# Performance work log

Hardware: AMD Instinct MI355X
Metric: run time of the kernel (lower is better)

Reference implementation:

```python
import jax, jax.numpy as jnp
import numpy as np

EMBED_DIM = 1024
NUM_HEADS = 16
HEAD_DIM = EMBED_DIM // NUM_HEADS  # 64
KV_RANK = 64
QK_RANK = 64
EPS = 1e-6


def rmsnorm(x, w):
    var = jnp.mean(x * x, axis=-1, keepdims=True)
    return x * jax.lax.rsqrt(var + EPS) * w


def setup_inputs() -> dict:
    key = jax.random.key(0)
    ks = jax.random.split(key, 6)
    B, N, C = 4, 2048, EMBED_DIM
    s = lambda fan_in: 1.0 / np.sqrt(fan_in)
    return {
        "x": jax.random.normal(ks[0], (B, N, C), dtype=jnp.float32),
        # nn.Linear weights stored as [out_features, in_features]
        "w_kv_a": jax.random.normal(ks[1], (KV_RANK, C), dtype=jnp.float32) * s(C),
        "w_kv_b": jax.random.normal(ks[2], (NUM_HEADS * HEAD_DIM * 2, KV_RANK), dtype=jnp.float32) * s(KV_RANK),
        "w_q_a": jax.random.normal(ks[3], (QK_RANK, C), dtype=jnp.float32) * s(C),
        "w_q_b": jax.random.normal(ks[4], (NUM_HEADS * HEAD_DIM, QK_RANK), dtype=jnp.float32) * s(QK_RANK),
        "w_proj": jax.random.normal(ks[5], (C, NUM_HEADS * HEAD_DIM), dtype=jnp.float32) * s(NUM_HEADS * HEAD_DIM),
        "kv_norm_w": jnp.ones((KV_RANK,), dtype=jnp.float32),
        "q_norm_w": jnp.ones((QK_RANK,), dtype=jnp.float32),
    }


def reference(x, w_kv_a, w_kv_b, w_q_a, w_q_b, w_proj, kv_norm_w, q_norm_w):
    B, N, C = x.shape
    H, D = NUM_HEADS, HEAD_DIM
    scale = D ** -0.5

    # low-rank KV path
    kv_latent = rmsnorm(x @ w_kv_a.T, kv_norm_w)              # [B,N,r]
    kv = (kv_latent @ w_kv_b.T).reshape(B, N, H, 2, D)
    k = kv[:, :, :, 0, :].transpose(0, 2, 1, 3)               # [B,H,N,D]
    v = kv[:, :, :, 1, :].transpose(0, 2, 1, 3)               # [B,H,N,D]

    # low-rank Q path
    q_latent = rmsnorm(x @ w_q_a.T, q_norm_w)                 # [B,N,r]
    q = (q_latent @ w_q_b.T).reshape(B, N, H, D).transpose(0, 2, 1, 3)

    attn = jnp.einsum("bhqd,bhkd->bhqk", q, k) * scale        # [B,H,N,N]
    attn = jax.nn.softmax(attn, axis=-1)
    y = jnp.einsum("bhqk,bhkd->bhqd", attn, v)                # [B,H,N,D]

    y = y.transpose(0, 2, 1, 3).reshape(B, N, H * D)
    return y @ w_proj.T
```

## Files before the change

kernel.cpp:

```cpp
#include <hip/hip_runtime.h>
#include <stdint.h>

typedef __bf16 bf16;
typedef __bf16 bf16x8 __attribute__((ext_vector_type(8)));
typedef __bf16 bf16x4 __attribute__((ext_vector_type(4)));
typedef float  f32x4  __attribute__((ext_vector_type(4)));

#define MFMA16(a,b,c) __builtin_amdgcn_mfma_f32_16x16x32_bf16((a),(b),(c),0,0,0)
#define LOG2E 1.44269504f

__device__ __forceinline__ void gl16(const bf16* g, bf16* l) {
  __builtin_amdgcn_global_load_lds((const __attribute__((address_space(1))) void*)g,
                                   (__attribute__((address_space(3))) void*)l, 16, 0, 0);
}

#define OFF_XB     0LL
#define OFF_WAB    8388608LL
#define OFF_WKVB   8519680LL
#define OFF_WQB    8650752LL
#define OFF_WPROJ  8716288LL
#define OFF_LATN   9764864LL
#define OFF_K      10813440LL
#define OFF_VT     19202048LL
#define OFF_Q      27590656LL
#define OFF_Y      35979264LL

__global__ __launch_bounds__(256) void k_convert(
    const float* __restrict__ x, const float* __restrict__ wkva, const float* __restrict__ wkvb,
    const float* __restrict__ wqa, const float* __restrict__ wqb, const float* __restrict__ wproj,
    bf16* __restrict__ ws)
{
  int64_t q = (int64_t)blockIdx.x * 256 + threadIdx.x;
  const float* src; bf16* dst;
  if (q < 2097152LL)      { src = x + 4*q;                          dst = ws + OFF_XB + 4*q; }
  else if (q < 2129920LL) { int64_t e = 4*(q - 2097152LL);
                            int row = (int)(e >> 10), col = (int)(e & 1023);
                            src = (row < 64) ? (wkva + ((int64_t)row << 10) + col)
                                             : (wqa + ((int64_t)(row - 64) << 10) + col);
                            dst = ws + OFF_WAB + e; }
  else if (q < 2162688LL) { int64_t j = q - 2129920LL; src = wkvb + 4*j; dst = ws + OFF_WKVB + 4*j; }
  else if (q < 2179072LL) { int64_t j = q - 2162688LL; src = wqb  + 4*j; dst = ws + OFF_WQB  + 4*j; }
  else if (q < 2441216LL) { int64_t j = q - 2179072LL; src = wproj+ 4*j; dst = ws + OFF_WPROJ+ 4*j; }
  else return;
  float4 v = *(const float4*)src;
  bf16x4 o; o.x = (bf16)v.x; o.y = (bf16)v.y; o.z = (bf16)v.z; o.w = (bf16)v.w;
  *(bf16x4*)dst = o;
}

__device__ __forceinline__ void gemm_core(
    const bf16* __restrict__ A, const bf16* __restrict__ B,
    int lda, int ldb, int K, int m0, int n0,
    bf16* As, bf16* Bs, f32x4 acc[4][4])
{
  const int tid = threadIdx.x, lane = tid & 63;
  const int wr = tid >> 7, wc = (tid >> 6) & 1;
  const int r0 = tid >> 3, c0 = (tid & 7) * 8;
  const int csw = (((tid & 7) ^ (r0 & 7)) * 8);
  const int fr = lane & 15, fg = lane >> 4;
#pragma unroll
  for (int mi = 0; mi < 4; mi++)
#pragma unroll
    for (int ni = 0; ni < 4; ni++) acc[mi][ni] = (f32x4){0.f, 0.f, 0.f, 0.f};
  for (int kt = 0; kt < K; kt += 64) {
#pragma unroll
    for (int p = 0; p < 4; p++) {
      int row = p * 32 + r0;
      gl16(A + (int64_t)(m0 + row) * lda + kt + csw, As + row * 64 + c0);
      gl16(B + (int64_t)(n0 + row) * ldb + kt + csw, Bs + row * 64 + c0);
    }
    __syncthreads();
#pragma unroll
    for (int kk = 0; kk < 2; kk++) {
      bf16x8 af[4], bfr[4];
#pragma unroll
      for (int i = 0; i < 4; i++) {
        af[i]  = *(const bf16x8*)(As + (wr * 64 + i * 16 + fr) * 64 + (((kk * 4 + fg) ^ (fr & 7)) * 8));
        bfr[i] = *(const bf16x8*)(Bs + (wc * 64 + i * 16 + fr) * 64 + (((kk * 4 + fg) ^ (fr & 7)) * 8));
      }
#pragma unroll
      for (int mi = 0; mi < 4; mi++)
#pragma unroll
        for (int ni = 0; ni < 4; ni++)
          acc[mi][ni] = MFMA16(af[mi], bfr[ni], acc[mi][ni]);
    }
    __syncthreads();
  }
}

__global__ __launch_bounds__(256, 2) void k_latent(
    const bf16* __restrict__ xb, const bf16* __restrict__ wab,
    const float* __restrict__ kvw, const float* __restrict__ qw,
    bf16* __restrict__ latn)
{
  __shared__ bf16 As[128 * 64], Bs[128 * 64];
  f32x4 acc[4][4];
  const int m0 = blockIdx.x * 128;
  gemm_core(xb, wab, 1024, 1024, 1024, m0, 0, As, Bs, acc);
  const int tid = threadIdx.x, lane = tid & 63, wr = tid >> 7, wc = (tid >> 6) & 1;
  const int fr = lane & 15, fg = lane >> 4;
  const float* nw = wc ? qw : kvw;
  float wv[4];
#pragma unroll
  for (int ni = 0; ni < 4; ni++) wv[ni] = nw[ni * 16 + fr];
#pragma unroll
  for (int mi = 0; mi < 4; mi++) {
    f32x4 ss;
#pragma unroll
    for (int r = 0; r < 4; r++) {
      float s = 0.f;
#pragma unroll
      for (int ni = 0; ni < 4; ni++) { float v = acc[mi][ni][r]; s += v * v; }
      ss[r] = s;
    }
#pragma unroll
    for (int mask = 1; mask < 16; mask <<= 1)
#pragma unroll
      for (int r = 0; r < 4; r++) ss[r] += __shfl_xor(ss[r], mask, 64);
    f32x4 sc;
#pragma unroll
    for (int r = 0; r < 4; r++) sc[r] = rsqrtf(ss[r] * (1.f / 64.f) + 1e-6f);
#pragma unroll
    for (int ni = 0; ni < 4; ni++)
#pragma unroll
      for (int r = 0; r < 4; r++) {
        int row = m0 + wr * 64 + mi * 16 + fg * 4 + r;
        latn[(int64_t)row * 128 + wc * 64 + ni * 16 + fr] = (bf16)(acc[mi][ni][r] * sc[r] * wv[ni]);
      }
  }
}

__global__ __launch_bounds__(256, 2) void k_kv(
    const bf16* __restrict__ latn, const bf16* __restrict__ wkvb,
    bf16* __restrict__ kb, bf16* __restrict__ vtb)
{
  __shared__ bf16 As[128 * 64], Bs[128 * 64];
  f32x4 acc[4][4];
  const int m0 = blockIdx.x * 128, h = blockIdx.y;
  gemm_core(latn, wkvb, 128, 64, 64, m0, h * 128, As, Bs, acc);
  const int tid = threadIdx.x, lane = tid & 63, wr = tid >> 7, wc = (tid >> 6) & 1;
  const int fr = lane & 15, fg = lane >> 4;
#pragma unroll
  for (int mi = 0; mi < 4; mi++)
#pragma unroll
    for (int ni = 0; ni < 4; ni++)
#pragma unroll
      for (int r = 0; r < 4; r++) {
        int m = m0 + wr * 64 + mi * 16 + fg * 4 + r;
        int b = m >> 11, t = m & 2047;
        int c = ni * 16 + fr;
        bf16 v = (bf16)acc[mi][ni][r];
        if (wc == 0) kb [(int64_t)((b * 16 + h) * 2048 + t) * 64 + c] = v;
        else         vtb[(int64_t)((b * 16 + h) * 64 + c) * 2048 + t] = v;
      }
}

__global__ __launch_bounds__(256, 2) void k_q(
    const bf16* __restrict__ latn, const bf16* __restrict__ wqb,
    bf16* __restrict__ qbuf)
{
  __shared__ bf16 As[128 * 64], Bs[128 * 64];
  f32x4 acc[4][4];
  const int m0 = blockIdx.x * 128, n0 = blockIdx.y * 128;
  gemm_core(latn + 64, wqb, 128, 64, 64, m0, n0, As, Bs, acc);
  const int tid = threadIdx.x, lane = tid & 63, wr = tid >> 7, wc = (tid >> 6) & 1;
  const int fr = lane & 15, fg = lane >> 4;
#pragma unroll
  for (int mi = 0; mi < 4; mi++)
#pragma unroll
    for (int ni = 0; ni < 4; ni++)
#pragma unroll
      for (int r = 0; r < 4; r++) {
        int m = m0 + wr * 64 + mi * 16 + fg * 4 + r;
        int b = m >> 11, t = m & 2047;
        int n = n0 + wc * 64 + ni * 16 + fr;
        int hh = n >> 6, d = n & 63;
        qbuf[(int64_t)((b * 16 + hh) * 2048 + t) * 64 + d] = (bf16)(acc[mi][ni][r] * 0.125f);
      }
}

__global__ __launch_bounds__(256, 2) void k_attn(
    const bf16* __restrict__ qb, const bf16* __restrict__ kb,
    const bf16* __restrict__ vtb, bf16* __restrict__ yb)
{
  __shared__ bf16 Vts[64 * 64];
  __shared__ bf16 KsP[128 * 64];
  const int bh = blockIdx.x, qt = blockIdx.y;
  const int b = bh >> 4, h = bh & 15;
  const int tid = threadIdx.x, lane = tid & 63, w = tid >> 6;
  const int fr = lane & 15, fg = lane >> 4;
  const int fg4 = fg * 4;
  const int64_t base = (int64_t)bh * (2048 * 64);
  bf16* Ks = KsP;
  bf16* Pw = KsP + w * 32 * 64;
  const int q0 = qt * 128 + w * 32;

  bf16x8 aq[2][2];
#pragma unroll
  for (int mi = 0; mi < 2; mi++)
#pragma unroll
    for (int kk = 0; kk < 2; kk++)
      aq[mi][kk] = *(const bf16x8*)(qb + base + (int64_t)(q0 + mi * 16 + fr) * 64 + kk * 32 + fg * 8);

  f32x4 o[2][4];
  float mS[2], lS[2];
#pragma unroll
  for (int mi = 0; mi < 2; mi++) {
#pragma unroll
    for (int di = 0; di < 4; di++) o[mi][di] = (f32x4){0.f, 0.f, 0.f, 0.f};
    mS[mi] = -__builtin_inff(); lS[mi] = 0.f;
  }
  const int srow = tid >> 3, scol = tid & 7;

  for (int kt = 0; kt < 32; kt++) {
    const int t0 = kt * 64;
#pragma unroll
    for (int p = 0; p < 2; p++) {
      int row = p * 32 + srow;
      int csw = ((scol ^ (row & 7)) * 8);
      gl16(kb  + base + (int64_t)(t0 + row) * 64 + csw, Ks  + row * 64 + scol * 8);
      gl16(vtb + base + (int64_t)row * 2048 + t0 + csw, Vts + row * 64 + scol * 8);
    }
    __syncthreads();
    f32x4 sT[2][4];
#pragma unroll
    for (int mi = 0; mi < 2; mi++)
#pragma unroll
      for (int ni = 0; ni < 4; ni++) sT[mi][ni] = (f32x4){0.f, 0.f, 0.f, 0.f};
#pragma unroll
    for (int kk = 0; kk < 2; kk++) {
      bf16x8 bk[4];
#pragma unroll
      for (int ni = 0; ni < 4; ni++)
        bk[ni] = *(const bf16x8*)(Ks + (ni * 16 + fr) * 64 + (((kk * 4 + fg) ^ (fr & 7)) * 8));
#pragma unroll
      for (int mi = 0; mi < 2; mi++)
#pragma unroll
        for (int ni = 0; ni < 4; ni++)
          sT[mi][ni] = MFMA16(bk[ni], aq[mi][kk], sT[mi][ni]);
    }
    __syncthreads();
#pragma unroll
    for (int mi = 0; mi < 2; mi++) {
      float pm = sT[mi][0][0];
#pragma unroll
      for (int ni = 0; ni < 4; ni++)
#pragma unroll
        for (int r = 0; r < 4; r++) pm = fmaxf(pm, sT[mi][ni][r]);
      pm = fmaxf(pm, __shfl_xor(pm, 16, 64));
      pm = fmaxf(pm, __shfl_xor(pm, 32, 64));
      const bool grew = __any(pm > mS[mi]);
      float alphaS = 1.f;
      if (grew) {
        float mn = fmaxf(mS[mi], pm);
        alphaS = exp2f((mS[mi] - mn) * LOG2E);
        mS[mi] = mn;
      }
      const float mnL = mS[mi] * LOG2E;
      float rs = 0.f;
      bf16* pwr = Pw + (mi * 16 + fr) * 64 + (fg & 1) * 4;
      const int cxor = fr & 7;
#pragma unroll
      for (int ni = 0; ni < 4; ni++) {
        float p0 = exp2f(fmaf(sT[mi][ni][0], LOG2E, -mnL));
        float p1 = exp2f(fmaf(sT[mi][ni][1], LOG2E, -mnL));
        float p2 = exp2f(fmaf(sT[mi][ni][2], LOG2E, -mnL));
        float p3 = exp2f(fmaf(sT[mi][ni][3], LOG2E, -mnL));
        rs += (p0 + p1) + (p2 + p3);
        bf16x4 pk4;
        pk4[0] = (bf16)p0; pk4[1] = (bf16)p1; pk4[2] = (bf16)p2; pk4[3] = (bf16)p3;
        *(bf16x4*)(pwr + (((ni * 2 + (fg >> 1)) ^ cxor) << 3)) = pk4;
      }
      rs += __shfl_xor(rs, 16, 64);
      rs += __shfl_xor(rs, 32, 64);
      if (grew) {
        lS[mi] = lS[mi] * alphaS + rs;
        float aO[4];
#pragma unroll
        for (int r = 0; r < 4; r++) aO[r] = __shfl(alphaS, fg4 + r, 64);
#pragma unroll
        for (int di = 0; di < 4; di++)
#pragma unroll
          for (int r = 0; r < 4; r++) o[mi][di][r] *= aO[r];
      } else {
        lS[mi] += rs;
      }
    }
#pragma unroll
    for (int k2 = 0; k2 < 2; k2++) {
      bf16x8 pa[2], vv[4];
#pragma unroll
      for (int mi = 0; mi < 2; mi++)
        pa[mi] = *(const bf16x8*)(Pw + (mi * 16 + fr) * 64 + (((k2 * 4 + fg) ^ (fr & 7)) * 8));
#pragma unroll
      for (int di = 0; di < 4; di++)
        vv[di] = *(const bf16x8*)(Vts + (di * 16 + fr) * 64 + (((k2 * 4 + fg) ^ (fr & 7)) * 8));
#pragma unroll
      for (int mi = 0; mi < 2; mi++)
#pragma unroll
        for (int di = 0; di < 4; di++)
          o[mi][di] = MFMA16(pa[mi], vv[di], o[mi][di]);
    }
    __syncthreads();
  }
#pragma unroll
  for (int mi = 0; mi < 2; mi++) {
    float lO[4];
#pragma unroll
    for (int r = 0; r < 4; r++) lO[r] = __shfl(lS[mi], fg4 + r, 64);
#pragma unroll
    for (int di = 0; di < 4; di++)
#pragma unroll
      for (int r = 0; r < 4; r++) {
        int t = q0 + mi * 16 + fg * 4 + r;
        float v = o[mi][di][r] / lO[r];
        yb[((int64_t)b * 2048 + t) * 1024 + h * 64 + di * 16 + fr] = (bf16)v;
      }
  }
}

__global__ __launch_bounds__(256, 2) void k_proj(
    const bf16* __restrict__ yb, const bf16* __restrict__ wp, float* __restrict__ out)
{
  __shared__ bf16 As[128 * 64], Bs[128 * 64];
  f32x4 acc[4][4];
  const int m0 = blockIdx.x * 128, n0 = blockIdx.y * 128;
  gemm_core(yb, wp, 1024, 1024, 1024, m0, n0, As, Bs, acc);
  const int tid = threadIdx.x, lane = tid & 63, wr = tid >> 7, wc = (tid >> 6) & 1;
  const int fr = lane & 15, fg = lane >> 4;
#pragma unroll
  for (int mi = 0; mi < 4; mi++)
#pragma unroll
    for (int ni = 0; ni < 4; ni++)
#pragma unroll
      for (int r = 0; r < 4; r++) {
        int m = m0 + wr * 64 + mi * 16 + fg * 4 + r;
        int n = n0 + wc * 64 + ni * 16 + fr;
        out[(int64_t)m * 1024 + n] = acc[mi][ni][r];
      }
}

extern "C" void kernel_launch(void* const* d_in, const int* in_sizes, int n_in,
                              void* d_out, int out_size, void* d_ws, size_t ws_size,
                              hipStream_t stream) {
  (void)in_sizes; (void)n_in; (void)out_size; (void)ws_size;
  const float* x     = (const float*)d_in[0];
  const float* wkva  = (const float*)d_in[1];
  const float* wkvb  = (const float*)d_in[2];
  const float* wqa   = (const float*)d_in[3];
  const float* wqb   = (const float*)d_in[4];
  const float* wproj = (const float*)d_in[5];
  const float* kvw   = (const float*)d_in[6];
  const float* qw    = (const float*)d_in[7];
  bf16* ws  = (bf16*)d_ws;
  float* out = (float*)d_out;

  k_convert<<<dim3(9536), dim3(256), 0, stream>>>(x, wkva, wkvb, wqa, wqb, wproj, ws);
  k_latent <<<dim3(64), dim3(256), 0, stream>>>(ws + OFF_XB, ws + OFF_WAB, kvw, qw, ws + OFF_LATN);
  k_kv     <<<dim3(64, 16), dim3(256), 0, stream>>>(ws + OFF_LATN, ws + OFF_WKVB, ws + OFF_K, ws + OFF_VT);
  k_q      <<<dim3(64, 8), dim3(256), 0, stream>>>(ws + OFF_LATN, ws + OFF_WQB, ws + OFF_Q);
  k_attn   <<<dim3(64, 16), dim3(256), 0, stream>>>(ws + OFF_Q, ws + OFF_K, ws + OFF_VT, ws + OFF_Y);
  k_proj   <<<dim3(64, 8), dim3(256), 0, stream>>>(ws + OFF_Y, ws + OFF_WPROJ, out);
}
```

Baseline: 305.0 us.

## Double-buffer K/V tiles in attention and widen blocks to 8 waves

The attention kernel now prefetches the next K and V^T tile into a second LDS buffer while computing on the current one. Each block has 512 threads covering 256 queries, so every K/V tile in LDS is shared by more query rows. The P scratch gets its own dedicated buffer instead of aliasing the K tile, which removes one barrier per iteration. The cost is higher LDS use per block (about 64KB) and fewer blocks in the grid, with launch bounds raised to 512 threads and 4 blocks per CU, which may not be reachable.

```diff
diff --git a/kernel.cpp b/kernel.cpp
--- a/kernel.cpp
+++ b/kernel.cpp
@@ -178,21 +178,31 @@
       }
 }
 
-__global__ __launch_bounds__(256, 2) void k_attn(
+__global__ __launch_bounds__(512, 4) void k_attn(
     const bf16* __restrict__ qb, const bf16* __restrict__ kb,
     const bf16* __restrict__ vtb, bf16* __restrict__ yb)
 {
-  __shared__ bf16 Vts[64 * 64];
-  __shared__ bf16 KsP[128 * 64];
+  __shared__ bf16 Ks[2][64 * 64];
+  __shared__ bf16 Vts[2][64 * 64];
+  __shared__ bf16 Ps[8][32 * 64];
   const int bh = blockIdx.x, qt = blockIdx.y;
   const int b = bh >> 4, h = bh & 15;
   const int tid = threadIdx.x, lane = tid & 63, w = tid >> 6;
   const int fr = lane & 15, fg = lane >> 4;
   const int fg4 = fg * 4;
   const int64_t base = (int64_t)bh * (2048 * 64);
-  bf16* Ks = KsP;
-  bf16* Pw = KsP + w * 32 * 64;
-  const int q0 = qt * 128 + w * 32;
+  bf16* Pw = Ps[w];
+  const int q0 = qt * 256 + w * 32;
+
+  const int srow = tid >> 3, scol = tid & 7;
+  const int csw = ((scol ^ (srow & 7)) * 8);
+  const bf16* kSrc = kb  + base + (int64_t)srow * 64   + csw;
+  const bf16* vSrc = vtb + base + (int64_t)srow * 2048 + csw;
+  bf16* kD[2] = { &Ks[0][tid * 8],  &Ks[1][tid * 8]  };
+  bf16* vD[2] = { &Vts[0][tid * 8], &Vts[1][tid * 8] };
+
+  gl16(kSrc, kD[0]);
+  gl16(vSrc, vD[0]);
 
   bf16x8 aq[2][2];
 #pragma unroll
@@ -209,18 +219,19 @@
     for (int di = 0; di < 4; di++) o[mi][di] = (f32x4){0.f, 0.f, 0.f, 0.f};
     mS[mi] = -__builtin_inff(); lS[mi] = 0.f;
   }
-  const int srow = tid >> 3, scol = tid & 7;
+
+  asm volatile("s_waitcnt vmcnt(0)" ::: "memory");
+  __builtin_amdgcn_s_barrier();
 
   for (int kt = 0; kt < 32; kt++) {
-    const int t0 = kt * 64;
-#pragma unroll
-    for (int p = 0; p < 2; p++) {
-      int row = p * 32 + srow;
-      int csw = ((scol ^ (row & 7)) * 8);
-      gl16(kb  + base + (int64_t)(t0 + row) * 64 + csw, Ks  + row * 64 + scol * 8);
-      gl16(vtb + base + (int64_t)row * 2048 + t0 + csw, Vts + row * 64 + scol * 8);
-    }
-    __syncthreads();
+    const int cur = kt & 1;
+    if (kt < 31) {
+      const int64_t t0n = (int64_t)(kt + 1) * 64;
+      gl16(kSrc + t0n * 64, kD[cur ^ 1]);
+      gl16(vSrc + t0n,      vD[cur ^ 1]);
+    }
+    const bf16* Kc = Ks[cur];
+    const bf16* Vc = Vts[cur];
     f32x4 sT[2][4];
 #pragma unroll
     for (int mi = 0; mi < 2; mi++)
@@ -231,14 +242,13 @@
       bf16x8 bk[4];
 #pragma unroll
       for (int ni = 0; ni < 4; ni++)
-        bk[ni] = *(const bf16x8*)(Ks + (ni * 16 + fr) * 64 + (((kk * 4 + fg) ^ (fr & 7)) * 8));
+        bk[ni] = *(const bf16x8*)(Kc + (ni * 16 + fr) * 64 + (((kk * 4 + fg) ^ (fr & 7)) * 8));
 #pragma unroll
       for (int mi = 0; mi < 2; mi++)
 #pragma unroll
         for (int ni = 0; ni < 4; ni++)
           sT[mi][ni] = MFMA16(bk[ni], aq[mi][kk], sT[mi][ni]);
     }
-    __syncthreads();
 #pragma unroll
     for (int mi = 0; mi < 2; mi++) {
       float pm = sT[mi][0][0];
@@ -293,14 +303,15 @@
         pa[mi] = *(const bf16x8*)(Pw + (mi * 16 + fr) * 64 + (((k2 * 4 + fg) ^ (fr & 7)) * 8));
 #pragma unroll
       for (int di = 0; di < 4; di++)
-        vv[di] = *(const bf16x8*)(Vts + (di * 16 + fr) * 64 + (((k2 * 4 + fg) ^ (fr & 7)) * 8));
+        vv[di] = *(const bf16x8*)(Vc + (di * 16 + fr) * 64 + (((k2 * 4 + fg) ^ (fr & 7)) * 8));
 #pragma unroll
       for (int mi = 0; mi < 2; mi++)
 #pragma unroll
         for (int di = 0; di < 4; di++)
           o[mi][di] = MFMA16(pa[mi], vv[di], o[mi][di]);
     }
-    __syncthreads();
+    asm volatile("s_waitcnt vmcnt(0)" ::: "memory");
+    __builtin_amdgcn_s_barrier();
   }
 #pragma unroll
   for (int mi = 0; mi < 2; mi++) {
@@ -358,6 +369,6 @@
   k_latent <<<dim3(64), dim3(256), 0, stream>>>(ws + OFF_XB, ws + OFF_WAB, kvw, qw, ws + OFF_LATN);
   k_kv     <<<dim3(64, 16), dim3(256), 0, stream>>>(ws + OFF_LATN, ws + OFF_WKVB, ws + OFF_K, ws + OFF_VT);
   k_q      <<<dim3(64, 8), dim3(256), 0, stream>>>(ws + OFF_LATN, ws + OFF_WQB, ws + OFF_Q);
-  k_attn   <<<dim3(64, 16), dim3(256), 0, stream>>>(ws + OFF_Q, ws + OFF_K, ws + OFF_VT, ws + OFF_Y);
+  k_attn   <<<dim3(64, 8), dim3(512), 0, stream>>>(ws + OFF_Q, ws + OFF_K, ws + OFF_VT, ws + OFF_Y);
   k_proj   <<<dim3(64, 8), dim3(256), 0, stream>>>(ws + OFF_Y, ws + OFF_WPROJ, out);
 }
```

After: 348.0 us. 1.14x slower.
